# Optimization experiments

Hardware: AMD Instinct MI355X
Metric: run time of the kernel (lower is better)

Reference implementation:

```python
import jax, jax.numpy as jnp
import numpy as np

N = 50000        # nodes
E = 800000       # edges (before self-loops)
IN = 128         # in_channels
HID = 32         # hidden_channels
HEADS = 8        # num_heads
G = 64           # num graphs in batch
NEG_SLOPE = 0.2  # PyG GATConv default


def setup_inputs() -> dict:
    key = jax.random.key(0)
    ks = jax.random.split(key, 12)
    x = jax.random.normal(ks[0], (N, IN), jnp.float32)
    edge_index = jax.random.randint(ks[1], (2, E), 0, N, jnp.int32)
    edge_attr = jax.random.normal(ks[2], (E, 4), jnp.float32)
    batch = jnp.sort(jax.random.randint(ks[3], (N,), 0, G, jnp.int32))
    s = 0.05
    # GATConv 1: in -> HEADS*HID
    W1 = jax.random.normal(ks[4], (IN, HEADS * HID), jnp.float32) * s
    a_src1 = jax.random.normal(ks[5], (HEADS, HID), jnp.float32) * s
    a_dst1 = jax.random.normal(ks[6], (HEADS, HID), jnp.float32) * s
    b1 = jnp.zeros((HEADS * HID,), jnp.float32)
    # GATConv 2: HEADS*HID -> HID (heads=1)
    W2 = jax.random.normal(ks[7], (HEADS * HID, HID), jnp.float32) * s
    a_src2 = jax.random.normal(ks[8], (1, HID), jnp.float32) * s
    a_dst2 = jax.random.normal(ks[9], (1, HID), jnp.float32) * s
    b2 = jnp.zeros((HID,), jnp.float32)
    return {"x": x, "edge_index": edge_index, "edge_attr": edge_attr, "batch": batch,
            "W1": W1, "a_src1": a_src1, "a_dst1": a_dst1, "b1": b1,
            "W2": W2, "a_src2": a_src2, "a_dst2": a_dst2, "b2": b2}


def gat_conv(x, src, dst, W, a_src, a_dst, b):
    # x: [N, F_in]; W: [F_in, H*C]; a_src/a_dst: [H, C]
    H, C = a_src.shape
    h = (x @ W).reshape(N, H, C)                      # [N, H, C]
    al_s = jnp.einsum('nhc,hc->nh', h, a_src)         # [N, H]
    al_d = jnp.einsum('nhc,hc->nh', h, a_dst)
    e = jax.nn.leaky_relu(al_s[src] + al_d[dst], NEG_SLOPE)  # [Etot, H]
    # segment softmax over incoming edges of each dst node
    m = jax.ops.segment_max(e, dst, num_segments=N)
    p = jnp.exp(e - m[dst])
    z = jax.ops.segment_sum(p, dst, num_segments=N)
    alpha = p / z[dst]                                # [Etot, H]
    out = jax.ops.segment_sum(alpha[:, :, None] * h[src], dst, num_segments=N)
    return out.reshape(N, H * C) + b


def reference(x, edge_index, edge_attr, batch, W1, a_src1, a_dst1, b1, W2, a_src2, a_dst2, b2):
    # edge_attr is ignored: GATConv was built without edge_dim (PyG lin_edge=None).
    loops = jnp.arange(N, dtype=edge_index.dtype)     # PyG add_self_loops=True
    src = jnp.concatenate([edge_index[0], loops])
    dst = jnp.concatenate([edge_index[1], loops])
    h = jax.nn.relu(gat_conv(x, src, dst, W1, a_src1, a_dst1, b1))
    # dropout p=0.2 is identity in eval mode
    h = gat_conv(h, src, dst, W2, a_src2, a_dst2, b2)  # [N, HID]
    # global_mean_pool over graph ids
    sums = jax.ops.segment_sum(h, batch, num_segments=G)
    cnts = jax.ops.segment_sum(jnp.ones((N, 1), h.dtype), batch, num_segments=G)
    return sums / jnp.maximum(cnts, 1.0)              # [G, HID]
```

## Files before the change

kernel.cpp:

```cpp
#include <hip/hip_runtime.h>
#include <hip/hip_bf16.h>

#define NNODES 50000
#define NEDGES 800000
#define FIN 128
#define HID 32
#define HEADS 8
#define NG 64
#define NEG_SLOPE 0.2f
#define MAXDEG 64
#define NPX 6250

using bf16x8 = __attribute__((ext_vector_type(8))) short;
using f32x4  = __attribute__((ext_vector_type(4))) float;
using f32x2  = __attribute__((ext_vector_type(2))) float;

static __device__ __forceinline__ float leaky(float x) {
    return x > 0.f ? x : NEG_SLOPE * x;
}
static __device__ __forceinline__ unsigned short f2bf(float f) {
    unsigned int x = __float_as_uint(f);
    return (unsigned short)((x + 0x7FFFu + ((x >> 16) & 1u)) >> 16);
}
static __device__ __forceinline__ unsigned int pack2bf(float lo, float hi) {
    return (unsigned int)f2bf(lo) | ((unsigned int)f2bf(hi) << 16);
}
static __device__ __forceinline__ float bfl(unsigned int u) {
    return __uint_as_float(u << 16);
}
static __device__ __forceinline__ float bfh(unsigned int u) {
    return __uint_as_float(u & 0xFFFF0000u);
}
static __device__ __forceinline__ unsigned char f2fp8(float f) {
    return (unsigned char)(__builtin_amdgcn_cvt_pk_fp8_f32(f, f, 0, false) & 0xFF);
}

#define ZERO_BLOCKS 196
__global__ void zero_swz_kernel(int* __restrict__ cnt,
                                const float* __restrict__ W1, const float* __restrict__ W2,
                                const float* __restrict__ a_src1, const float* __restrict__ a_dst1,
                                unsigned short* __restrict__ w1s,
                                unsigned short* __restrict__ w2s,
                                unsigned short* __restrict__ w1al) {
    if (blockIdx.x < ZERO_BLOCKS) {
        int i = blockIdx.x * 256 + threadIdx.x;
        if (i < NNODES) cnt[i] = 0;
        return;
    }
    int idx = (blockIdx.x - ZERO_BLOCKS) * 256 + threadIdx.x;
    if (idx < 32768) {
        int j    = idx & 7;
        int lane = (idx >> 3) & 63;
        int ks   = (idx >> 9) & 3;
        int ct   = idx >> 11;
        int k = ks * 32 + (lane >> 4) * 8 + j;
        int n = ct * 16 + (lane & 15);
        w1s[idx] = f2bf(W1[k * 256 + n]);
    } else if (idx < 32768 + 8192) {
        int id2  = idx - 32768;
        int j    = id2 & 7;
        int lane = (id2 >> 3) & 63;
        int ks   = (id2 >> 9) & 7;
        int ct   = id2 >> 12;
        int k = ks * 32 + (lane >> 4) * 8 + j;
        int n = ct * 16 + (lane & 15);
        w2s[id2] = f2bf(W2[k * 32 + n]);
    } else if (idx < 32768 + 8192 + 2048) {
        int id3  = idx - 40960;
        int j    = id3 & 7;
        int lane = (id3 >> 3) & 63;
        int ks   = id3 >> 9;
        int k = ks * 32 + (lane >> 4) * 8 + j;
        int c = lane & 15;
        int h = c & 7;
        const float* av = (c < 8) ? a_src1 : a_dst1;
        float v = 0.f;
#pragma unroll 8
        for (int cc = 0; cc < 32; ++cc)
            v += W1[k * 256 + h * 32 + cc] * av[h * 32 + cc];
        w1al[id3] = f2bf(v);
    }
}

#define SCAT_GROUPS 782
__global__ void scatter_kernel(const int* __restrict__ ei, int* __restrict__ cnt,
                               unsigned short* __restrict__ csr) {
    int xcd = blockIdx.x & 7;
    int slice = blockIdx.x >> 3;
    int e4 = slice * 256 + threadIdx.x;
    int dlo = xcd * NPX;
    int dhi = dlo + NPX;
    if (e4 < NEDGES / 4) {
        int4 d = *(const int4*)(ei + NEDGES + e4 * 4);
        int4 s;
        bool a0 = d.x >= dlo && d.x < dhi;
        bool a1 = d.y >= dlo && d.y < dhi;
        bool a2 = d.z >= dlo && d.z < dhi;
        bool a3 = d.w >= dlo && d.w < dhi;
        if (a0 | a1 | a2 | a3) s = *(const int4*)(ei + e4 * 4);
        if (a0) { int p = atomicAdd(&cnt[d.x], 1); csr[(d.x << 6) + p] = (unsigned short)s.x; }
        if (a1) { int p = atomicAdd(&cnt[d.y], 1); csr[(d.y << 6) + p] = (unsigned short)s.y; }
        if (a2) { int p = atomicAdd(&cnt[d.z], 1); csr[(d.z << 6) + p] = (unsigned short)s.z; }
        if (a3) { int p = atomicAdd(&cnt[d.w], 1); csr[(d.w << 6) + p] = (unsigned short)s.w; }
    }
}

__global__ __launch_bounds__(256) void gemm1_mfma_kernel(const float* __restrict__ x,
                                                         const unsigned short* __restrict__ w1s,
                                                         const unsigned short* __restrict__ w1al,
                                                         unsigned char* __restrict__ h1f8,
                                                         float* __restrict__ al_s,
                                                         float* __restrict__ al_d) {
    int t = threadIdx.x;
    int w = t >> 6;
    int l = t & 63;
    int lane16 = l & 15, quad = l >> 4;

    bf16x8 bf[4][4];
    const bf16x8* wp = (const bf16x8*)w1s;
#pragma unroll
    for (int ct = 0; ct < 4; ++ct)
#pragma unroll
        for (int ks = 0; ks < 4; ++ks)
            bf[ct][ks] = wp[((w * 4 + ct) * 4 + ks) * 64 + l];

    bf16x8 bf_al[4];
    if (w == 0) {
        const bf16x8* ap = (const bf16x8*)w1al;
#pragma unroll
        for (int ks = 0; ks < 4; ++ks)
            bf_al[ks] = ap[ks * 64 + l];
    }

    int rbase = blockIdx.x * 64;
    for (int rg = 0; rg < 4; ++rg) {
        int row0 = rbase + rg * 16;
        int r = row0 + lane16;
        int r_eff = r < NNODES ? r : NNODES - 1;
        bf16x8 af[4];
#pragma unroll
        for (int ks = 0; ks < 4; ++ks) {
            const float* ap = x + (size_t)r_eff * FIN + ks * 32 + quad * 8;
            float4 a0 = *(const float4*)ap;
            float4 a1 = *(const float4*)(ap + 4);
            bf16x8 v;
            v[0] = (short)f2bf(a0.x); v[1] = (short)f2bf(a0.y);
            v[2] = (short)f2bf(a0.z); v[3] = (short)f2bf(a0.w);
            v[4] = (short)f2bf(a1.x); v[5] = (short)f2bf(a1.y);
            v[6] = (short)f2bf(a1.z); v[7] = (short)f2bf(a1.w);
            af[ks] = v;
        }
        f32x4 acc[4];
#pragma unroll
        for (int ct = 0; ct < 4; ++ct) acc[ct] = (f32x4){0.f, 0.f, 0.f, 0.f};
#pragma unroll
        for (int ks = 0; ks < 4; ++ks)
#pragma unroll
            for (int ct = 0; ct < 4; ++ct)
                acc[ct] = __builtin_amdgcn_mfma_f32_16x16x32_bf16(af[ks], bf[ct][ks], acc[ct], 0, 0, 0);

        if (w == 0) {
            f32x4 aal = (f32x4){0.f, 0.f, 0.f, 0.f};
#pragma unroll
            for (int ks = 0; ks < 4; ++ks)
                aal = __builtin_amdgcn_mfma_f32_16x16x32_bf16(af[ks], bf_al[ks], aal, 0, 0, 0);
#pragma unroll
            for (int reg = 0; reg < 4; ++reg) {
                int gr = row0 + quad * 4 + reg;
                if (gr < NNODES) {
                    if (lane16 < 8) al_s[gr * HEADS + lane16] = aal[reg];
                    else            al_d[gr * HEADS + lane16 - 8] = aal[reg];
                }
            }
        }

#pragma unroll
        for (int ct = 0; ct < 4; ++ct)
#pragma unroll
            for (int reg = 0; reg < 4; ++reg) {
                int gr = row0 + quad * 4 + reg;
                if (gr < NNODES)
                    h1f8[(size_t)gr * 256 + w * 64 + ct * 16 + lane16] = f2fp8(acc[ct][reg]);
            }
    }
}

#define G1_SLICES 782
__global__ __launch_bounds__(256) void gather1_kernel(const unsigned char* __restrict__ h1f8,
                                                      const float* __restrict__ al_s,
                                                      const float* __restrict__ al_d,
                                                      const int* __restrict__ cnt,
                                                      const unsigned short* __restrict__ csr,
                                                      const float* __restrict__ b1,
                                                      unsigned short* __restrict__ out1b) {
    int b = blockIdx.x;
    int xcd = b & 7;
    int slice = b >> 3;
    int t = threadIdx.x;
    int l = t & 63;
    int q = l & 31;
    int base = l & 32;
    int ln = slice * 8 + (t >> 5);
    if (ln >= NPX) return;
    int n = xcd * NPX + ln;
    int e_st = q >> 3;
    int h_st = q & 7;
    int h_f  = q >> 2;
    float ad_st = al_d[n * HEADS + h_st];

    float p = __expf(leaky(al_s[n * HEADS + h_f] + al_d[n * HEADS + h_f]));
    float z = p;
    f32x2 acc01, acc23, acc45, acc67;
    {
        uint2 v = *(const uint2*)(h1f8 + (size_t)n * 256 + q * 8);
        f32x2 pp = (f32x2){p, p};
        acc01 = pp * __builtin_amdgcn_cvt_pk_f32_fp8(v.x, false);
        acc23 = pp * __builtin_amdgcn_cvt_pk_f32_fp8(v.x, true);
        acc45 = pp * __builtin_amdgcn_cvt_pk_f32_fp8(v.y, false);
        acc67 = pp * __builtin_amdgcn_cvt_pk_f32_fp8(v.y, true);
    }

    int beg = n << 6;
    int dg  = cnt[n];
    int end = beg + dg;
    int   sc0 = n, sc1 = n;
    float pc0 = 0.f, pc1 = 0.f;
    if (e_st < dg) {
        sc0 = csr[beg + e_st];
        pc0 = __expf(leaky(al_s[sc0 * HEADS + h_st] + ad_st));
    }
    if (e_st + 4 < dg) {
        sc1 = csr[beg + 4 + e_st];
        pc1 = __expf(leaky(al_s[sc1 * HEADS + h_st] + ad_st));
    }
    for (int i = beg; i < end; i += 8) {
        int remn = end - (i + 8);
        int   sn0 = n, sn1 = n;
        float pn0 = 0.f, pn1 = 0.f;
        if (e_st < remn) {
            sn0 = csr[i + 8 + e_st];
            pn0 = __expf(leaky(al_s[sn0 * HEADS + h_st] + ad_st));
        }
        if (e_st + 4 < remn) {
            sn1 = csr[i + 12 + e_st];
            pn1 = __expf(leaky(al_s[sn1 * HEADS + h_st] + ad_st));
        }
#pragma unroll
        for (int j = 0; j < 8; ++j) {
            int   sj  = (j < 4) ? __shfl(sc0, base + j * 8)
                                : __shfl(sc1, base + (j - 4) * 8);
            float pej = (j < 4) ? __shfl(pc0, base + j * 8 + h_f)
                                : __shfl(pc1, base + (j - 4) * 8 + h_f);
            uint2 v = *(const uint2*)(h1f8 + (size_t)sj * 256 + q * 8);
            z += pej;
            f32x2 pj = (f32x2){pej, pej};
            acc01 += pj * __builtin_amdgcn_cvt_pk_f32_fp8(v.x, false);
            acc23 += pj * __builtin_amdgcn_cvt_pk_f32_fp8(v.x, true);
            acc45 += pj * __builtin_amdgcn_cvt_pk_f32_fp8(v.y, false);
            acc67 += pj * __builtin_amdgcn_cvt_pk_f32_fp8(v.y, true);
        }
        sc0 = sn0; pc0 = pn0; sc1 = sn1; pc1 = pn1;
    }
    float inv = 1.0f / z;
    float4 b0 = *(const float4*)(b1 + q * 8);
    float4 b2 = *(const float4*)(b1 + q * 8 + 4);
    float o[8];
    o[0] = acc01[0] * inv + b0.x; o[1] = acc01[1] * inv + b0.y;
    o[2] = acc23[0] * inv + b0.z; o[3] = acc23[1] * inv + b0.w;
    o[4] = acc45[0] * inv + b2.x; o[5] = acc45[1] * inv + b2.y;
    o[6] = acc67[0] * inv + b2.z; o[7] = acc67[1] * inv + b2.w;
#pragma unroll
    for (int k = 0; k < 8; ++k) o[k] = o[k] > 0.f ? o[k] : 0.f;
    uint4 pk;
    pk.x = pack2bf(o[0], o[1]); pk.y = pack2bf(o[2], o[3]);
    pk.z = pack2bf(o[4], o[5]); pk.w = pack2bf(o[6], o[7]);
    *(uint4*)(out1b + (size_t)n * 256 + q * 8) = pk;
}

__global__ __launch_bounds__(256) void gemm2_mfma_kernel(const unsigned short* __restrict__ out1b,
                                                         const unsigned short* __restrict__ w2s,
                                                         const float* __restrict__ a_src,
                                                         const float* __restrict__ a_dst,
                                                         unsigned short* __restrict__ h2b,
                                                         float* __restrict__ al_s,
                                                         float* __restrict__ al_d) {
    int t = threadIdx.x;
    int w = t >> 6;
    int l = t & 63;
    int lane16 = l & 15, quad = l >> 4;

    bf16x8 bf[2][8];
    const bf16x8* wp = (const bf16x8*)w2s;
#pragma unroll
    for (int ct = 0; ct < 2; ++ct)
#pragma unroll
        for (int ks = 0; ks < 8; ++ks)
            bf[ct][ks] = wp[((ct * 8 + ks)) * 64 + l];

    float as_c[2], ad_c[2];
#pragma unroll
    for (int ct = 0; ct < 2; ++ct) {
        as_c[ct] = a_src[ct * 16 + lane16];
        ad_c[ct] = a_dst[ct * 16 + lane16];
    }

    int row0 = blockIdx.x * 64 + w * 16;
    int r = row0 + lane16;
    int r_eff = r < NNODES ? r : NNODES - 1;
    f32x4 acc[2];
    acc[0] = (f32x4){0.f, 0.f, 0.f, 0.f};
    acc[1] = (f32x4){0.f, 0.f, 0.f, 0.f};
#pragma unroll
    for (int ks = 0; ks < 8; ++ks) {
        bf16x8 af = *(const bf16x8*)(out1b + (size_t)r_eff * 256 + ks * 32 + quad * 8);
        acc[0] = __builtin_amdgcn_mfma_f32_16x16x32_bf16(af, bf[0][ks], acc[0], 0, 0, 0);
        acc[1] = __builtin_amdgcn_mfma_f32_16x16x32_bf16(af, bf[1][ks], acc[1], 0, 0, 0);
    }
#pragma unroll
    for (int reg = 0; reg < 4; ++reg) {
        int gr = row0 + quad * 4 + reg;
        if (gr < NNODES) {
            h2b[(size_t)gr * 32 + lane16]      = f2bf(acc[0][reg]);
            h2b[(size_t)gr * 32 + 16 + lane16] = f2bf(acc[1][reg]);
        }
        float ps = acc[0][reg] * as_c[0] + acc[1][reg] * as_c[1];
        float pd = acc[0][reg] * ad_c[0] + acc[1][reg] * ad_c[1];
#pragma unroll
        for (int m = 1; m < 16; m <<= 1) {
            ps += __shfl_xor(ps, m);
            pd += __shfl_xor(pd, m);
        }
        if (lane16 == 0 && gr < NNODES) {
            al_s[gr] = ps;
            al_d[gr] = pd;
        }
    }
}

#define G2_SLICES 391
__global__ __launch_bounds__(256) void gather2_kernel(const unsigned short* __restrict__ h2b,
                                                      const float* __restrict__ al_s,
                                                      const float* __restrict__ al_d,
                                                      const int* __restrict__ cnt,
                                                      const unsigned short* __restrict__ csr,
                                                      const float* __restrict__ b2,
                                                      float* __restrict__ out2) {
    int b = blockIdx.x;
    int xcd = b & 7;
    int slice = b >> 3;
    int t = threadIdx.x;
    int l = t & 63;
    int e_sl = l & 15;
    int base = l & 48;
    int c0 = (l & 15) * 2;
    int ln = slice * 16 + (t >> 4);
    if (ln >= NPX) return;
    int n = xcd * NPX + ln;

    float ad = al_d[n];
    float p = __expf(leaky(al_s[n] + ad));
    float z = p;
    float acc0, acc1;
    {
        unsigned int v = *(const unsigned int*)(h2b + (size_t)n * HID + c0);
        acc0 = p * bfl(v);
        acc1 = p * bfh(v);
    }
    int beg = n << 6;
    int dg  = cnt[n];
    int end = beg + dg;
    int   src_c = n;
    float pe_c  = 0.f;
    if (e_sl < dg) {
        src_c = csr[beg + e_sl];
        pe_c = __expf(leaky(al_s[src_c] + ad));
    }
    for (int i = beg; i < end; i += 16) {
        int remn = end - (i + 16);
        int   src_n = n;
        float pe_n  = 0.f;
        if (e_sl < remn) {
            src_n = csr[i + 16 + e_sl];
            pe_n = __expf(leaky(al_s[src_n] + ad));
        }
        int m = end - i < 16 ? end - i : 16;
        for (int j0 = 0; j0 < m; j0 += 8) {
#pragma unroll
            for (int jj = 0; jj < 8; ++jj) {
                int   sj  = __shfl(src_c, base + j0 + jj);
                float pej = __shfl(pe_c, base + j0 + jj);
                unsigned int v = *(const unsigned int*)(h2b + (size_t)sj * HID + c0);
                z += pej;
                acc0 += pej * bfl(v);
                acc1 += pej * bfh(v);
            }
        }
        src_c = src_n; pe_c = pe_n;
    }
    float inv = 1.0f / z;
    float2 o;
    o.x = acc0 * inv + b2[c0];
    o.y = acc1 * inv + b2[c0 + 1];
    *(float2*)(out2 + (size_t)n * HID + c0) = o;
}

__global__ __launch_bounds__(256) void pool_kernel(const float* __restrict__ out2,
                                                   const int* __restrict__ batch,
                                                   float* __restrict__ out) {
    __shared__ float red[256];
    int g = blockIdx.x;
    int t = threadIdx.x;
    int c = t & 31;
    int sub = t >> 5;
    int beg, end;
    {
        int lo = 0, hi = NNODES;
        while (lo < hi) { int mid = (lo + hi) >> 1; if (batch[mid] < g) lo = mid + 1; else hi = mid; }
        beg = lo;
        lo = beg; hi = NNODES;
        while (lo < hi) { int mid = (lo + hi) >> 1; if (batch[mid] < g + 1) lo = mid + 1; else hi = mid; }
        end = lo;
    }
    float s = 0.f;
    for (int n = beg + sub; n < end; n += 8) s += out2[n * HID + c];
    red[t] = s;
    __syncthreads();
    if (t < 32) {
        float tot = 0.f;
#pragma unroll
        for (int k = 0; k < 8; ++k) tot += red[c + 32 * k];
        int cnt2 = end - beg;
        out[g * HID + c] = tot / (float)(cnt2 > 0 ? cnt2 : 1);
    }
}

extern "C" void kernel_launch(void* const* d_in, const int* in_sizes, int n_in,
                              void* d_out, int out_size, void* d_ws, size_t ws_size,
                              hipStream_t stream) {
    const float* x      = (const float*)d_in[0];
    const int*   ei     = (const int*)d_in[1];
    const int*   batch  = (const int*)d_in[3];
    const float* W1     = (const float*)d_in[4];
    const float* a_src1 = (const float*)d_in[5];
    const float* a_dst1 = (const float*)d_in[6];
    const float* b1     = (const float*)d_in[7];
    const float* W2     = (const float*)d_in[8];
    const float* a_src2 = (const float*)d_in[9];
    const float* a_dst2 = (const float*)d_in[10];
    const float* b2     = (const float*)d_in[11];
    float* out = (float*)d_out;

    char* ws = (char*)d_ws;
    size_t off = 0;
    auto alloc = [&](size_t bytes) {
        size_t o = off;
        off = (off + bytes + 255) & ~(size_t)255;
        return o;
    };
    unsigned char*  h1f8  = (unsigned char*)(ws + alloc((size_t)NNODES * 256));
    unsigned short* out1b = (unsigned short*)(ws + alloc((size_t)NNODES * 256 * 2));
    unsigned short* h2b   = (unsigned short*)(ws + alloc((size_t)NNODES * HID * 2));
    unsigned short* w1s   = (unsigned short*)(ws + alloc((size_t)16 * 4 * 64 * 8 * 2));
    unsigned short* w2s   = (unsigned short*)(ws + alloc((size_t)2 * 8 * 64 * 8 * 2));
    unsigned short* w1al  = (unsigned short*)(ws + alloc((size_t)4 * 64 * 8 * 2));
    float* out2   = (float*)(ws + alloc((size_t)NNODES * HID * 4));
    float* al_s1  = (float*)(ws + alloc((size_t)NNODES * HEADS * 4));
    float* al_d1  = (float*)(ws + alloc((size_t)NNODES * HEADS * 4));
    float* al_s2  = (float*)(ws + alloc((size_t)NNODES * 4));
    float* al_d2  = (float*)(ws + alloc((size_t)NNODES * 4));
    int*   cnt    = (int*)(ws + alloc((size_t)NNODES * 4));
    unsigned short* csr = (unsigned short*)(ws + alloc((size_t)NNODES * MAXDEG * 2));
    (void)ws_size;

    zero_swz_kernel<<<ZERO_BLOCKS + 168, 256, 0, stream>>>(cnt, W1, W2, a_src1, a_dst1,
                                                           w1s, w2s, w1al);
    scatter_kernel<<<SCAT_GROUPS * 8, 256, 0, stream>>>(ei, cnt, csr);

    gemm1_mfma_kernel<<<(NNODES + 63) / 64, 256, 0, stream>>>(x, w1s, w1al,
                                                              h1f8, al_s1, al_d1);
    gather1_kernel<<<8 * G1_SLICES, 256, 0, stream>>>(h1f8, al_s1, al_d1, cnt, csr, b1, out1b);

    gemm2_mfma_kernel<<<(NNODES + 63) / 64, 256, 0, stream>>>(out1b, w2s, a_src2, a_dst2,
                                                              h2b, al_s2, al_d2);
    gather2_kernel<<<8 * G2_SLICES, 256, 0, stream>>>(h2b, al_s2, al_d2, cnt, csr, b2, out2);
    pool_kernel<<<NG, 256, 0, stream>>>(out2, batch, out);
}
```

Before: 251.4 us.

## Fuse mean-pool into gather2 via atomics and zero buffers with memset

The second gather kernel now adds each node's output straight into a per-graph accumulator with float atomicAdd, so the out2 buffer and the pool kernel's pass over it are gone. A small finalize kernel divides by the per-graph node counts. The counter and accumulator zeroing moves to hipMemsetAsync, and the weight-swizzle kernel loses its zeroing blocks. With only 64 graphs and sorted batch ids, about 50000 nodes × 32 channels of atomics hit 2048 addresses, so contention is heavy, and float atomics make the sums order-nondeterministic.

```diff
diff --git a/kernel.cpp b/kernel.cpp
--- a/kernel.cpp
+++ b/kernel.cpp
@@ -35,19 +35,12 @@
     return (unsigned char)(__builtin_amdgcn_cvt_pk_fp8_f32(f, f, 0, false) & 0xFF);
 }
 
-#define ZERO_BLOCKS 196
-__global__ void zero_swz_kernel(int* __restrict__ cnt,
-                                const float* __restrict__ W1, const float* __restrict__ W2,
-                                const float* __restrict__ a_src1, const float* __restrict__ a_dst1,
-                                unsigned short* __restrict__ w1s,
-                                unsigned short* __restrict__ w2s,
-                                unsigned short* __restrict__ w1al) {
-    if (blockIdx.x < ZERO_BLOCKS) {
-        int i = blockIdx.x * 256 + threadIdx.x;
-        if (i < NNODES) cnt[i] = 0;
-        return;
-    }
-    int idx = (blockIdx.x - ZERO_BLOCKS) * 256 + threadIdx.x;
+__global__ void swz_kernel(const float* __restrict__ W1, const float* __restrict__ W2,
+                           const float* __restrict__ a_src1, const float* __restrict__ a_dst1,
+                           unsigned short* __restrict__ w1s,
+                           unsigned short* __restrict__ w2s,
+                           unsigned short* __restrict__ w1al) {
+    int idx = blockIdx.x * 256 + threadIdx.x;
     if (idx < 32768) {
         int j    = idx & 7;
         int lane = (idx >> 3) & 63;
@@ -344,7 +337,8 @@
                                                       const int* __restrict__ cnt,
                                                       const unsigned short* __restrict__ csr,
                                                       const float* __restrict__ b2,
-                                                      float* __restrict__ out2) {
+                                                      const int* __restrict__ batch,
+                                                      float* __restrict__ poolacc) {
     int b = blockIdx.x;
     int xcd = b & 7;
     int slice = b >> 3;
@@ -398,20 +392,19 @@
         src_c = src_n; pe_c = pe_n;
     }
     float inv = 1.0f / z;
-    float2 o;
-    o.x = acc0 * inv + b2[c0];
-    o.y = acc1 * inv + b2[c0 + 1];
-    *(float2*)(out2 + (size_t)n * HID + c0) = o;
-}
-
-__global__ __launch_bounds__(256) void pool_kernel(const float* __restrict__ out2,
-                                                   const int* __restrict__ batch,
-                                                   float* __restrict__ out) {
-    __shared__ float red[256];
-    int g = blockIdx.x;
-    int t = threadIdx.x;
-    int c = t & 31;
-    int sub = t >> 5;
+    float o0 = acc0 * inv + b2[c0];
+    float o1 = acc1 * inv + b2[c0 + 1];
+    int g = batch[n];
+    atomicAdd(&poolacc[g * HID + c0], o0);
+    atomicAdd(&poolacc[g * HID + c0 + 1], o1);
+}
+
+__global__ __launch_bounds__(256) void finalize_kernel(const float* __restrict__ poolacc,
+                                                       const int* __restrict__ batch,
+                                                       float* __restrict__ out) {
+    int idx = blockIdx.x * 256 + threadIdx.x;
+    if (idx >= NG * HID) return;
+    int g = idx >> 5;
     int beg, end;
     {
         int lo = 0, hi = NNODES;
@@ -421,17 +414,8 @@
         while (lo < hi) { int mid = (lo + hi) >> 1; if (batch[mid] < g + 1) lo = mid + 1; else hi = mid; }
         end = lo;
     }
-    float s = 0.f;
-    for (int n = beg + sub; n < end; n += 8) s += out2[n * HID + c];
-    red[t] = s;
-    __syncthreads();
-    if (t < 32) {
-        float tot = 0.f;
-#pragma unroll
-        for (int k = 0; k < 8; ++k) tot += red[c + 32 * k];
-        int cnt2 = end - beg;
-        out[g * HID + c] = tot / (float)(cnt2 > 0 ? cnt2 : 1);
-    }
+    int c = end - beg;
+    out[idx] = poolacc[idx] / (float)(c > 0 ? c : 1);
 }
 
 extern "C" void kernel_launch(void* const* d_in, const int* in_sizes, int n_in,
@@ -463,17 +447,18 @@
     unsigned short* w1s   = (unsigned short*)(ws + alloc((size_t)16 * 4 * 64 * 8 * 2));
     unsigned short* w2s   = (unsigned short*)(ws + alloc((size_t)2 * 8 * 64 * 8 * 2));
     unsigned short* w1al  = (unsigned short*)(ws + alloc((size_t)4 * 64 * 8 * 2));
-    float* out2   = (float*)(ws + alloc((size_t)NNODES * HID * 4));
     float* al_s1  = (float*)(ws + alloc((size_t)NNODES * HEADS * 4));
     float* al_d1  = (float*)(ws + alloc((size_t)NNODES * HEADS * 4));
     float* al_s2  = (float*)(ws + alloc((size_t)NNODES * 4));
     float* al_d2  = (float*)(ws + alloc((size_t)NNODES * 4));
-    int*   cnt    = (int*)(ws + alloc((size_t)NNODES * 4));
+    size_t zbeg = alloc((size_t)NNODES * 4 + (size_t)NG * HID * 4);
+    int*   cnt     = (int*)(ws + zbeg);
+    float* poolacc = (float*)(ws + zbeg + (size_t)NNODES * 4);
     unsigned short* csr = (unsigned short*)(ws + alloc((size_t)NNODES * MAXDEG * 2));
     (void)ws_size;
 
-    zero_swz_kernel<<<ZERO_BLOCKS + 168, 256, 0, stream>>>(cnt, W1, W2, a_src1, a_dst1,
-                                                           w1s, w2s, w1al);
+    hipMemsetAsync(ws + zbeg, 0, (size_t)NNODES * 4 + (size_t)NG * HID * 4, stream);
+    swz_kernel<<<168, 256, 0, stream>>>(W1, W2, a_src1, a_dst1, w1s, w2s, w1al);
     scatter_kernel<<<SCAT_GROUPS * 8, 256, 0, stream>>>(ei, cnt, csr);
 
     gemm1_mfma_kernel<<<(NNODES + 63) / 64, 256, 0, stream>>>(x, w1s, w1al,
@@ -482,6 +467,7 @@
 
     gemm2_mfma_kernel<<<(NNODES + 63) / 64, 256, 0, stream>>>(out1b, w2s, a_src2, a_dst2,
                                                               h2b, al_s2, al_d2);
-    gather2_kernel<<<8 * G2_SLICES, 256, 0, stream>>>(h2b, al_s2, al_d2, cnt, csr, b2, out2);
-    pool_kernel<<<NG, 256, 0, stream>>>(out2, batch, out);
-}
+    gather2_kernel<<<8 * G2_SLICES, 256, 0, stream>>>(h2b, al_s2, al_d2, cnt, csr, b2,
+                                                      batch, poolacc);
+    finalize_kernel<<<8, 256, 0, stream>>>(poolacc, batch, out);
+}
```

Result: slower. 396.7 us (+57.8%).
